# Kernel optimization log

Measured on AMD Instinct MI355X. Metric: run time of the kernel, lower is better.

## Reference

```python
import jax, jax.numpy as jnp
import numpy as np

B, T, D, H, C = 128, 256, 256, 1024, 10


def setup_inputs() -> dict:
    key = jax.random.key(0)
    ks = jax.random.split(key, 11)
    std = 1.0 / T  # matches nn.init.normal_(std=1/seq_length)
    inp = {
        'x':   jax.random.normal(ks[0], (B, T, D), dtype=jnp.float32),
        'Wfx': jax.random.normal(ks[1], (D, H), dtype=jnp.float32) * std,
        'Wix': jax.random.normal(ks[2], (D, H), dtype=jnp.float32) * std,
        'Wgx': jax.random.normal(ks[3], (D, H), dtype=jnp.float32) * std,
        'Wox': jax.random.normal(ks[4], (D, H), dtype=jnp.float32) * std,
        'Wfh': jax.random.normal(ks[5], (H, H), dtype=jnp.float32) * std,
        'Wih': jax.random.normal(ks[6], (H, H), dtype=jnp.float32) * std,
        'Wgh': jax.random.normal(ks[7], (H, H), dtype=jnp.float32) * std,
        'Woh': jax.random.normal(ks[8], (H, H), dtype=jnp.float32) * std,
        'bf':  jnp.zeros((H,), jnp.float32),
        'bi':  jnp.zeros((H,), jnp.float32),
        'bg':  jnp.zeros((H,), jnp.float32),
        'bo':  jnp.zeros((H,), jnp.float32),
        'Wph': jax.random.normal(ks[9], (H, C), dtype=jnp.float32) * std,
        'bp':  jnp.zeros((C,), jnp.float32),
    }
    return inp


def reference(x, Wfx, Wix, Wgx, Wox, Wfh, Wih, Wgh, Woh, bf, bi, bg, bo, Wph, bp):
    b, t, d = x.shape
    h = Wfh.shape[0]
    # Fuse the 4 input-side and 4 hidden-side matmuls into two big GEMMs per step
    Wx = jnp.concatenate([Wfx, Wix, Wgx, Wox], axis=1)  # [D, 4H]
    Wh = jnp.concatenate([Wfh, Wih, Wgh, Woh], axis=1)  # [H, 4H]
    bb = jnp.concatenate([bf, bi, bg, bo])              # [4H]

    # Precompute all input projections in one batched GEMM: [T, B, 4H]
    xg = jnp.einsum('btd,dk->tbk', x, Wx) + bb

    def step(carry, xgt):
        hs, cs = carry
        gates = xgt + hs @ Wh  # [B, 4H]
        f = jax.nn.sigmoid(gates[:, 0 * h:1 * h])
        i = jax.nn.sigmoid(gates[:, 1 * h:2 * h])
        g = jnp.tanh(gates[:, 2 * h:3 * h])
        o = jax.nn.sigmoid(gates[:, 3 * h:4 * h])
        cs = g * i + cs * f
        hs = jnp.tanh(cs) * o
        return (hs, cs), None

    h0 = jnp.zeros((b, h), x.dtype)
    c0 = jnp.zeros((b, h), x.dtype)
    (hT, _), _ = jax.lax.scan(step, (h0, c0), xg)
    return hT @ Wph + bp
```

## Files before the change

kernel.cpp:

```cpp
#include <hip/hip_runtime.h>
#include <math.h>


#define BB 128
#define TT 256
#define DD 256
#define HH 1024
#define NKT 40
#define KHT 20
#define PF 4

typedef __bf16 bf16x8 __attribute__((ext_vector_type(8)));
typedef float  f32x4  __attribute__((ext_vector_type(4)));
typedef unsigned short u16;
typedef u16 u16x8 __attribute__((ext_vector_type(8)));

__device__ __forceinline__ u16 f2bf(float f){
  unsigned u = __builtin_bit_cast(unsigned, f);
  u += 0x7fffu + ((u >> 16) & 1u);
  return (u16)(u >> 16);
}
__device__ __forceinline__ float bf2f(u16 b){
  unsigned u = ((unsigned)b) << 16;
  return __builtin_bit_cast(float, u);
}

__global__ void prep_wpack(const float* __restrict__ Wfx, const float* __restrict__ Wix,
                           const float* __restrict__ Wgx, const float* __restrict__ Wox,
                           const float* __restrict__ Wfh, const float* __restrict__ Wih,
                           const float* __restrict__ Wgh, const float* __restrict__ Woh,
                           u16* __restrict__ Wpack){
  int id = blockIdx.x * 256 + threadIdx.x;
  int lane = id & 63;
  int kt = (id >> 6) % NKT;
  int ct = id / (64 * NKT);
  int col = ct * 16 + (lane & 15);
  int g = col >> 10, n = col & 1023;
  int kbase = kt * 32 + (lane >> 4) * 8;
  const float* Wx = (g==0) ? Wfx : (g==1) ? Wix : (g==2) ? Wgx : Wox;
  const float* Wh = (g==0) ? Wfh : (g==1) ? Wih : (g==2) ? Wgh : Woh;
  u16x8 v;
  #pragma unroll
  for (int j = 0; j < 8; ++j){
    int k = kbase + j;
    float f = (k < DD) ? Wx[k * HH + n] : Wh[(k - DD) * HH + n];
    v[j] = f2bf(f);
  }
  *(u16x8*)(Wpack + (size_t)id * 8) = v;
}

__global__ void prep_xT(const float* __restrict__ x, u16* __restrict__ xT){
  int id = blockIdx.x * 256 + threadIdx.x;
  int t = id >> 12;
  int b = (id >> 5) & 127;
  int d0 = (id & 31) * 8;
  const float* src = x + ((size_t)b * TT + t) * DD + d0;
  u16x8 v;
  #pragma unroll
  for (int j = 0; j < 8; ++j) v[j] = f2bf(src[j]);
  *(u16x8*)(xT + (size_t)id * 8) = v;
}

__global__ __launch_bounds__(512) void lstm_step(
    const u16* __restrict__ xTt,
    const u16* __restrict__ Wpack,
    const u16* __restrict__ hin,
    u16* __restrict__ hout,
    float* __restrict__ cbuf,
    const float* __restrict__ bfv, const float* __restrict__ biv,
    const float* __restrict__ bgv, const float* __restrict__ bov){
  __shared__ u16x8 As4[NKT * 64];
  __shared__ float gLds[16][132];
  __shared__ float pLds[16][132];
  const int tid = threadIdx.x;
  const int n0 = blockIdx.x * 32;
  const int m0 = blockIdx.y * 16;

  const int w = tid >> 6, lane = tid & 63, cr = lane & 15, q4 = lane >> 4;
  const int g  = w & 3;
  const int kh = w >> 2;
  const int ktBeg = kh * KHT;

  const size_t ct0 = (size_t)(g * 64 + blockIdx.x * 2);
  const u16x8* Wp = (const u16x8*)Wpack;
  const u16x8* wq0 = Wp + ct0 * NKT * 64 + lane;
  const u16x8* wq1 = wq0 + NKT * 64;

  u16x8 aP[PF], b0P[PF], b1P[PF];
  #pragma unroll
  for (int i = 0; i < PF; ++i){
    b0P[i] = wq0[(size_t)(ktBeg + i) * 64];
    b1P[i] = wq1[(size_t)(ktBeg + i) * 64];
  }

  #pragma unroll
  for (int it = 0; it < 5; ++it){
    int ch = tid + it * 512;
    int m = ch / 160;
    int k0 = (ch - m * 160) * 8;
    const u16* src = (k0 < DD) ? (xTt + (m0 + m) * DD + k0)
                               : (hin + (m0 + m) * HH + (k0 - DD));
    u16x8 val = *(const u16x8*)src;
    int kt = k0 >> 5, q = (k0 >> 3) & 3;
    As4[kt * 64 + 16 * q + m] = val;
  }
  __syncthreads();

  #pragma unroll
  for (int i = 0; i < PF; ++i) aP[i] = As4[(ktBeg + i) * 64 + lane];

  f32x4 acc0 = {0.f, 0.f, 0.f, 0.f}, acc1 = {0.f, 0.f, 0.f, 0.f};
  #pragma unroll
  for (int kt = 0; kt < KHT; ++kt){
    const int slot = kt & (PF - 1);
    u16x8 ac = aP[slot], b0 = b0P[slot], b1 = b1P[slot];
    if (kt + PF < KHT){
      aP[slot]  = As4[(ktBeg + kt + PF) * 64 + lane];
      b0P[slot] = wq0[(size_t)(ktBeg + kt + PF) * 64];
      b1P[slot] = wq1[(size_t)(ktBeg + kt + PF) * 64];
    }
    acc0 = __builtin_amdgcn_mfma_f32_16x16x32_bf16(__builtin_bit_cast(bf16x8, ac),
             __builtin_bit_cast(bf16x8, b0), acc0, 0, 0, 0);
    acc1 = __builtin_amdgcn_mfma_f32_16x16x32_bf16(__builtin_bit_cast(bf16x8, ac),
             __builtin_bit_cast(bf16x8, b1), acc1, 0, 0, 0);
  }

  if (kh){
    #pragma unroll
    for (int r = 0; r < 4; ++r){
      pLds[q4 * 4 + r][g * 32 + cr]      = acc0[r];
      pLds[q4 * 4 + r][g * 32 + 16 + cr] = acc1[r];
    }
  }
  __syncthreads();
  if (!kh){
    const float* bptr = (g==0) ? bfv : (g==1) ? biv : (g==2) ? bgv : bov;
    float bias0 = bptr[n0 + cr], bias1 = bptr[n0 + 16 + cr];
    #pragma unroll
    for (int r = 0; r < 4; ++r){
      gLds[q4 * 4 + r][g * 32 + cr] =
          acc0[r] + pLds[q4 * 4 + r][g * 32 + cr] + bias0;
      gLds[q4 * 4 + r][g * 32 + 16 + cr] =
          acc1[r] + pLds[q4 * 4 + r][g * 32 + 16 + cr] + bias1;
    }
  }
  __syncthreads();

  {
    int row = tid >> 5, nn = tid & 31;
    float fp = gLds[row][nn],      ip = gLds[row][32 + nn];
    float gp = gLds[row][64 + nn], op = gLds[row][96 + nn];
    float fs = 1.f / (1.f + expf(-fp));
    float is = 1.f / (1.f + expf(-ip));
    float gs = tanhf(gp);
    float os = 1.f / (1.f + expf(-op));
    int gi = (m0 + row) * HH + n0 + nn;
    float cn = gs * is + cbuf[gi] * fs;
    cbuf[gi] = cn;
    hout[gi] = f2bf(tanhf(cn) * os);
  }
}

__global__ void final_proj(const u16* __restrict__ h, const float* __restrict__ Wph,
                           const float* __restrict__ bp, float* __restrict__ out){
  __shared__ float red[10][256];
  int b = blockIdx.x, tid = threadIdx.x;
  float p[10];
  #pragma unroll
  for (int c = 0; c < 10; ++c) p[c] = 0.f;
  for (int k = tid; k < HH; k += 256){
    float hv = bf2f(h[b * HH + k]);
    const float* wr = Wph + (size_t)k * 10;
    #pragma unroll
    for (int c = 0; c < 10; ++c) p[c] += hv * wr[c];
  }
  #pragma unroll
  for (int c = 0; c < 10; ++c) red[c][tid] = p[c];
  __syncthreads();
  for (int s = 128; s > 0; s >>= 1){
    if (tid < s){
      #pragma unroll
      for (int c = 0; c < 10; ++c) red[c][tid] += red[c][tid + s];
    }
    __syncthreads();
  }
  if (tid < 10) out[b * 10 + tid] = red[tid][0] + bp[tid];
}

extern "C" void kernel_launch(void* const* d_in, const int* in_sizes, int n_in,
                              void* d_out, int out_size, void* d_ws, size_t ws_size,
                              hipStream_t stream){
  (void)in_sizes; (void)n_in; (void)out_size; (void)ws_size;
  const float* x   = (const float*)d_in[0];
  const float* Wfx = (const float*)d_in[1];
  const float* Wix = (const float*)d_in[2];
  const float* Wgx = (const float*)d_in[3];
  const float* Wox = (const float*)d_in[4];
  const float* Wfh = (const float*)d_in[5];
  const float* Wih = (const float*)d_in[6];
  const float* Wgh = (const float*)d_in[7];
  const float* Woh = (const float*)d_in[8];
  const float* bfv = (const float*)d_in[9];
  const float* biv = (const float*)d_in[10];
  const float* bgv = (const float*)d_in[11];
  const float* bov = (const float*)d_in[12];
  const float* Wph = (const float*)d_in[13];
  const float* bp  = (const float*)d_in[14];

  char* ws = (char*)d_ws;
  u16*  Wpack = (u16*)ws;
  u16*  xT    = (u16*)(ws + 10485760);
  u16*  h0    = (u16*)(ws + 27262976);
  u16*  h1    = (u16*)(ws + 27525120);
  float* cb   = (float*)(ws + 27787264);

  prep_wpack<<<2560, 256, 0, stream>>>(Wfx, Wix, Wgx, Wox, Wfh, Wih, Wgh, Woh, Wpack);
  prep_xT<<<4096, 256, 0, stream>>>(x, xT);
  hipMemsetAsync(h0, 0, 262144, stream);
  hipMemsetAsync(cb, 0, 524288, stream);

  for (int t = 0; t < TT; ++t){
    const u16* hin = (t & 1) ? h1 : h0;
    u16*       hout = (t & 1) ? h0 : h1;
    lstm_step<<<dim3(32, 8), 512, 0, stream>>>(xT + (size_t)t * BB * DD, Wpack,
                                               hin, hout, cb, bfv, biv, bgv, bov);
  }
  final_proj<<<128, 256, 0, stream>>>(h0, Wph, bp, (float*)d_out);
}
```

Measured before the change: 1.984 ms.

## Swizzle LDS A tiles, deepen weight prefetch, hoist cell load, fast activations

Stores the A operand tile in LDS under an XOR swizzle so that lanes in the MFMA reads hit fewer bank conflicts. Prefetch depth for weights from global memory becomes five while the LDS operand stays at four. The previous cell state is loaded at kernel start so its latency overlaps the GEMM, and expf/tanhf are replaced by __expf-based sigmoid and tanh. The extra prefetch slots use more registers, and the fast activations lose some precision. The staging loop also carries a dead computation and an early break.

Result: no change. 1.951 ms (-1.6%).

```diff
diff --git a/kernel.cpp b/kernel.cpp
--- a/kernel.cpp
+++ b/kernel.cpp
@@ -8,7 +8,8 @@
 #define HH 1024
 #define NKT 40
 #define KHT 20
-#define PF 4
+#define PFA 4
+#define PFB 5
 
 typedef __bf16 bf16x8 __attribute__((ext_vector_type(8)));
 typedef float  f32x4  __attribute__((ext_vector_type(4)));
@@ -23,6 +24,15 @@
 __device__ __forceinline__ float bf2f(u16 b){
   unsigned u = ((unsigned)b) << 16;
   return __builtin_bit_cast(float, u);
+}
+__device__ __forceinline__ float sigm(float x){
+  return 1.f / (1.f + __expf(-x));
+}
+__device__ __forceinline__ float tanh_fast(float x){
+  return 2.f / (1.f + __expf(-2.f * x)) - 1.f;
+}
+__device__ __forceinline__ int swzb(int slot){
+  return slot ^ ((slot >> 6) & 7) ^ (((slot >> 4) & 3) << 1);
 }
 
 __global__ void prep_wpack(const float* __restrict__ Wfx, const float* __restrict__ Wix,
@@ -76,6 +86,10 @@
   const int n0 = blockIdx.x * 32;
   const int m0 = blockIdx.y * 16;
 
+  const int crow = tid >> 5, cnn = tid & 31;
+  const int gi = (m0 + crow) * HH + n0 + cnn;
+  const float cprev = cbuf[gi];
+
   const int w = tid >> 6, lane = tid & 63, cr = lane & 15, q4 = lane >> 4;
   const int g  = w & 3;
   const int kh = w >> 2;
@@ -86,38 +100,40 @@
   const u16x8* wq0 = Wp + ct0 * NKT * 64 + lane;
   const u16x8* wq1 = wq0 + NKT * 64;
 
-  u16x8 aP[PF], b0P[PF], b1P[PF];
-  #pragma unroll
-  for (int i = 0; i < PF; ++i){
+  u16x8 aP[PFA], b0P[PFB], b1P[PFB];
+  #pragma unroll
+  for (int i = 0; i < PFB; ++i){
     b0P[i] = wq0[(size_t)(ktBeg + i) * 64];
     b1P[i] = wq1[(size_t)(ktBeg + i) * 64];
   }
 
   #pragma unroll
-  for (int it = 0; it < 5; ++it){
-    int ch = tid + it * 512;
+  for (int it = 0; it < 10; ++it){
+    int ch = tid + it * 256;
+    ch = tid + it * 512;
+    if (it >= 5) break;
     int m = ch / 160;
     int k0 = (ch - m * 160) * 8;
     const u16* src = (k0 < DD) ? (xTt + (m0 + m) * DD + k0)
                                : (hin + (m0 + m) * HH + (k0 - DD));
     u16x8 val = *(const u16x8*)src;
     int kt = k0 >> 5, q = (k0 >> 3) & 3;
-    As4[kt * 64 + 16 * q + m] = val;
-  }
-  __syncthreads();
-
-  #pragma unroll
-  for (int i = 0; i < PF; ++i) aP[i] = As4[(ktBeg + i) * 64 + lane];
+    As4[swzb(kt * 64 + 16 * q + m)] = val;
+  }
+  __syncthreads();
+
+  #pragma unroll
+  for (int i = 0; i < PFA; ++i) aP[i] = As4[swzb((ktBeg + i) * 64 + lane)];
 
   f32x4 acc0 = {0.f, 0.f, 0.f, 0.f}, acc1 = {0.f, 0.f, 0.f, 0.f};
   #pragma unroll
   for (int kt = 0; kt < KHT; ++kt){
-    const int slot = kt & (PF - 1);
-    u16x8 ac = aP[slot], b0 = b0P[slot], b1 = b1P[slot];
-    if (kt + PF < KHT){
-      aP[slot]  = As4[(ktBeg + kt + PF) * 64 + lane];
-      b0P[slot] = wq0[(size_t)(ktBeg + kt + PF) * 64];
-      b1P[slot] = wq1[(size_t)(ktBeg + kt + PF) * 64];
+    u16x8 ac = aP[kt % PFA], b0 = b0P[kt % PFB], b1 = b1P[kt % PFB];
+    if (kt + PFA < KHT)
+      aP[kt % PFA] = As4[swzb((ktBeg + kt + PFA) * 64 + lane)];
+    if (kt + PFB < KHT){
+      b0P[kt % PFB] = wq0[(size_t)(ktBeg + kt + PFB) * 64];
+      b1P[kt % PFB] = wq1[(size_t)(ktBeg + kt + PFB) * 64];
     }
     acc0 = __builtin_amdgcn_mfma_f32_16x16x32_bf16(__builtin_bit_cast(bf16x8, ac),
              __builtin_bit_cast(bf16x8, b0), acc0, 0, 0, 0);
@@ -147,17 +163,15 @@
   __syncthreads();
 
   {
-    int row = tid >> 5, nn = tid & 31;
-    float fp = gLds[row][nn],      ip = gLds[row][32 + nn];
-    float gp = gLds[row][64 + nn], op = gLds[row][96 + nn];
-    float fs = 1.f / (1.f + expf(-fp));
-    float is = 1.f / (1.f + expf(-ip));
-    float gs = tanhf(gp);
-    float os = 1.f / (1.f + expf(-op));
-    int gi = (m0 + row) * HH + n0 + nn;
-    float cn = gs * is + cbuf[gi] * fs;
+    float fp = gLds[crow][cnn],      ip = gLds[crow][32 + cnn];
+    float gp = gLds[crow][64 + cnn], op = gLds[crow][96 + cnn];
+    float fs = sigm(fp);
+    float is = sigm(ip);
+    float gs = tanh_fast(gp);
+    float os = sigm(op);
+    float cn = gs * is + cprev * fs;
     cbuf[gi] = cn;
-    hout[gi] = f2bf(tanhf(cn) * os);
+    hout[gi] = f2bf(tanh_fast(cn) * os);
   }
 }
 
@@ -220,7 +234,7 @@
   hipMemsetAsync(cb, 0, 524288, stream);
 
   for (int t = 0; t < TT; ++t){
-    const u16* hin = (t & 1) ? h1 : h0;
+    const u16* hin  = (t & 1) ? h1 : h0;
     u16*       hout = (t & 1) ? h0 : h1;
     lstm_step<<<dim3(32, 8), 512, 0, stream>>>(xT + (size_t)t * BB * DD, Wpack,
                                                hin, hout, cb, bfv, biv, bgv, bov);
```
